# Optimization experiments

Measured on AMD Instinct MI355X. Metric: run time of the kernel, lower is better.

## Reference

```python
import jax, jax.numpy as jnp
import numpy as np

B, N, D, F, L, R = 16, 1024, 256, 128, 2, 2


def setup_inputs() -> dict:
    key = jax.random.key(0)
    ks = jax.random.split(key, 12)
    s = 0.05
    return {
        "node_embed": jax.random.normal(ks[0], (B, N, D), jnp.float32),
        "input_x": jax.random.normal(ks[1], (B, F), jnp.float32),
        "adj": jax.random.randint(ks[2], (R, B, N, N), 0, 2, jnp.int32),
        "WQi_w": jax.random.normal(ks[3], (L, F, F), jnp.float32) * s,
        "WQi_b": jnp.zeros((L, F), jnp.float32),
        "WQ_w": jax.random.normal(ks[4], (L, D + F, D), jnp.float32) * s,
        "WQ_b": jnp.zeros((L, D), jnp.float32),
        "WK_w": jax.random.normal(ks[5], (L, R, D + F, D), jnp.float32) * s,
        "WK_b": jnp.zeros((L, R, D), jnp.float32),
        "WV_w": jax.random.normal(ks[6], (L, R, D + F, D), jnp.float32) * s,
        "WV_b": jnp.zeros((L, R, D), jnp.float32),
        "WF_w": jax.random.normal(ks[7], (L, R * D, D), jnp.float32) * s,
        "WF_b": jnp.zeros((L, D), jnp.float32),
        "ln_g": jnp.ones((L, D), jnp.float32),
        "ln_b": jnp.zeros((L, D), jnp.float32),
    }


def _layer_norm(x, g, b, eps=1e-5):
    mu = jnp.mean(x, axis=-1, keepdims=True)
    var = jnp.var(x, axis=-1, keepdims=True)
    return (x - mu) * jax.lax.rsqrt(var + eps) * g + b


def reference(node_embed, input_x, adj, WQi_w, WQi_b, WQ_w, WQ_b,
              WK_w, WK_b, WV_w, WV_b, WF_w, WF_b, ln_g, ln_b):
    scale = 1.0 / (D ** 0.5)
    h = node_embed
    for l in range(L):
        # input feature projection, broadcast over nodes
        x1 = input_x @ WQi_w[l] + WQi_b[l]              # (B, F)
        x1 = jnp.broadcast_to(x1[:, None, :], (h.shape[0], h.shape[1], F))
        qc = jnp.concatenate([h, x1], axis=-1)          # (B, N, D+F)
        q = qc @ WQ_w[l] + WQ_b[l]                      # (B, N, D)
        outs = []
        for r in range(R):
            k = qc @ WK_w[l, r] + WK_b[l, r]            # (B, N, D)
            v = qc @ WV_w[l, r] + WV_b[l, r]            # (B, N, D)
            scores = jnp.einsum('bnd,bmd->bnm', q, k) * scale
            scores = jnp.where(adj[r] == 0, -1e9, scores)
            alpha = jax.nn.softmax(scores, axis=-1)
            outs.append(jnp.einsum('bnm,bmd->bnd', alpha, v))
        h_concat = jnp.concatenate(outs, axis=-1)       # (B, N, R*D)
        h_fused = jax.nn.relu(h_concat @ WF_w[l] + WF_b[l])
        h = _layer_norm(h + h_fused, ln_g[l], ln_b[l])
    return h
```

## Files before the change

### kernel.cpp

```cpp
#include <hip/hip_runtime.h>
#include <hip/hip_bf16.h>

#define BB 16
#define NN 1024
#define DD 256
#define FF_ 128
#define LL 2
#define RR 2
#define DF 384
#define MM (BB*NN)
#define NPROJ 1280
#define PK 768

typedef __attribute__((ext_vector_type(8))) short s16x8;
typedef __attribute__((ext_vector_type(4))) float f32x4;
typedef __attribute__((ext_vector_type(16))) float f32x16;
typedef __attribute__((ext_vector_type(2))) unsigned int u32x2;
typedef __attribute__((ext_vector_type(4))) unsigned int u32x4;
typedef __attribute__((ext_vector_type(4))) unsigned short us16x4;

__device__ __forceinline__ unsigned short f2bf(float f){
  unsigned u = __builtin_bit_cast(unsigned, f);
  u += 0x7fff + ((u >> 16) & 1);
  return (unsigned short)(u >> 16);
}

__device__ __forceinline__ void gload16(const void* g, void* l){
  __builtin_amdgcn_global_load_lds(
      (const __attribute__((address_space(1))) unsigned int*)g,
      (__attribute__((address_space(3))) unsigned int*)l, 16, 0, 0);
}

#define MFMA16(a,b,c) __builtin_amdgcn_mfma_f32_16x16x32_bf16((a),(b),(c),0,0,0)
#define MFMA32(a,b,c) __builtin_amdgcn_mfma_f32_32x32x16_bf16((a),(b),(c),0,0,0)

__global__ __launch_bounds__(256) void pack_adj(const int* __restrict__ adj,
                                                unsigned long long* __restrict__ bits){
  int w = threadIdx.x >> 6, lane = threadIdx.x & 63;
  size_t row = (size_t)blockIdx.x * 4 + w;
  const int* a = adj + row * NN;
  unsigned long long* brow = bits + row * 16;
  #pragma unroll
  for (int j = 0; j < 16; ++j){
    unsigned long long m = __ballot(a[j*64 + lane] != 0);
    if (lane == 0) brow[j] = m;
  }
}

#define PREP_WT   3840
#define PREP_WTF  1024
#define PREP_BALL 10
#define PREP_X1   16
#define PREP_H    2048
#define PREP_TOT  (PREP_WT+PREP_WTF+PREP_BALL+PREP_X1+PREP_H)

__global__ __launch_bounds__(256) void prep(
    const float* __restrict__ node, const float* __restrict__ inx,
    const float* __restrict__ WQi_w, const float* __restrict__ WQi_b,
    const float* __restrict__ WQ_w, const float* __restrict__ WK_w,
    const float* __restrict__ WV_w, const float* __restrict__ WQ_b,
    const float* __restrict__ WK_b, const float* __restrict__ WV_b,
    const float* __restrict__ WF_w,
    unsigned short* __restrict__ wtall, unsigned short* __restrict__ wtf,
    float* __restrict__ ball, unsigned short* __restrict__ x1bf,
    unsigned short* __restrict__ hbf){
  int bid = blockIdx.x, t = threadIdx.x;
  if (bid < PREP_WT){
    int o = bid*256 + t;
    int l = o / (NPROJ*DF); int oo = o - l*(NPROJ*DF);
    int n = oo / DF, k = oo - n*DF;
    const float* WQ = WQ_w + (size_t)l*DF*256;
    const float* WK = WK_w + (size_t)l*RR*DF*256;
    const float* WV = WV_w + (size_t)l*RR*DF*256;
    float v;
    if (n < 256)      v = WQ[(size_t)k*256 + n];
    else if (n < 768) v = WK[(size_t)((n-256)>>8)*(DF*256) + (size_t)k*256 + ((n-256)&255)];
    else              v = WV[(size_t)((n-768)>>8)*(DF*256) + (size_t)k*256 + ((n-768)&255)];
    wtall[o] = f2bf(v);
  } else if (bid < PREP_WT + PREP_WTF){
    int o = (bid - PREP_WT)*256 + t;
    int l = o >> 17; int oo = o & 131071;
    int n = oo >> 9, k = oo & 511;
    wtf[o] = f2bf(WF_w[(size_t)l*512*256 + (size_t)k*256 + n]);
  } else if (bid < PREP_WT + PREP_WTF + PREP_BALL){
    int o = (bid - PREP_WT - PREP_WTF)*256 + t;
    if (o < 2*NPROJ){
      int l = o / NPROJ, n = o - l*NPROJ;
      float v = (n < 256) ? WQ_b[l*256 + n]
              : (n < 768) ? WK_b[(size_t)l*512 + (n-256)]
                          : WV_b[(size_t)l*512 + (n-768)];
      ball[o] = v;
    }
  } else if (bid < PREP_WT + PREP_WTF + PREP_BALL + PREP_X1){
    int o = (bid - PREP_WT - PREP_WTF - PREP_BALL)*256 + t;
    int l = o >> 11, bj = o & 2047;
    int b = bj >> 7, j = bj & 127;
    const float* w = WQi_w + (size_t)l*FF_*FF_;
    float s = WQi_b[l*FF_ + j];
    for (int i = 0; i < FF_; ++i) s += inx[b*FF_ + i] * w[i*FF_ + j];
    x1bf[o] = f2bf(s);
  } else {
    int o = (bid - (PREP_TOT - PREP_H))*256 + t;
    const float4* src = (const float4*)node + (size_t)o*2;
    float4 a = src[0], c = src[1];
    uint4 pk;
    pk.x = (unsigned)f2bf(a.x) | ((unsigned)f2bf(a.y) << 16);
    pk.y = (unsigned)f2bf(a.z) | ((unsigned)f2bf(a.w) << 16);
    pk.z = (unsigned)f2bf(c.x) | ((unsigned)f2bf(c.y) << 16);
    pk.w = (unsigned)f2bf(c.z) | ((unsigned)f2bf(c.w) << 16);
    *(uint4*)(hbf + (size_t)o*8) = pk;
  }
}

__global__ __launch_bounds__(256) void gemm_big(const unsigned short* __restrict__ hbf,
    const unsigned short* __restrict__ x1l, const unsigned short* __restrict__ Wt,
    const float* __restrict__ bias, unsigned short* __restrict__ POUT,
    unsigned short* __restrict__ vtall){
  __shared__ unsigned short As[2][128*32];
  __shared__ unsigned short Bs[2][128*32];
  int t = threadIdx.x, lane = t & 63, w = t >> 6;
  int wr = w >> 1, wc = w & 1, l15 = lane & 15, lhi = lane >> 4;
  int bm = blockIdx.x, bn = blockIdx.y, bb = bm >> 3;
  f32x4 acc[4][4];
  #pragma unroll
  for (int m = 0; m < 4; ++m)
    #pragma unroll
    for (int n = 0; n < 4; ++n) acc[m][n] = (f32x4){0.f,0.f,0.f,0.f};

  auto STAGE = [&](int bi, int kk){
    #pragma unroll
    for (int i = 0; i < 2; ++i){
      int base = w*2048 + i*1024;
      int off = base + lane*16;
      int row = off >> 6, cb = off & 63;
      const char* asrc = (kk < 8)
        ? (const char*)hbf + ((size_t)(bm*128 + row)*256 + kk*32)*2 + cb
        : (const char*)x1l + ((size_t)bb*128 + (kk-8)*32)*2 + cb;
      gload16(asrc, (char*)As[bi] + base);
      gload16((const char*)Wt + ((size_t)(bn*128 + row)*DF + kk*32)*2 + cb,
              (char*)Bs[bi] + base);
    }
  };

  STAGE(0, 0);
  __syncthreads();
  for (int kk = 0; kk < 12; ++kk){
    int cur = kk & 1;
    if (kk + 1 < 12) STAGE(cur ^ 1, kk + 1);
    s16x8 af[4], bfr[4];
    #pragma unroll
    for (int m = 0; m < 4; ++m) af[m]  = *(const s16x8*)&As[cur][(wr*64 + m*16 + l15)*32 + lhi*8];
    #pragma unroll
    for (int n = 0; n < 4; ++n) bfr[n] = *(const s16x8*)&Bs[cur][(wc*64 + n*16 + l15)*32 + lhi*8];
    __builtin_amdgcn_s_setprio(1);
    #pragma unroll
    for (int m = 0; m < 4; ++m)
      #pragma unroll
      for (int n = 0; n < 4; ++n)
        acc[m][n] = MFMA16(af[m], bfr[n], acc[m][n]);
    __builtin_amdgcn_s_setprio(0);
    __syncthreads();
  }

  if (bn < 6){
    #pragma unroll
    for (int n = 0; n < 4; ++n){
      int gn = bn*128 + wc*64 + n*16 + l15;
      float bv = bias[gn];
      #pragma unroll
      for (int m = 0; m < 4; ++m){
        int gm = bm*128 + wr*64 + m*16 + lhi*4;
        #pragma unroll
        for (int i = 0; i < 4; ++i)
          POUT[(size_t)(gm + i)*PK + gn] = f2bf(acc[m][n][i] + bv);
      }
    }
  } else {
    #pragma unroll
    for (int n = 0; n < 4; ++n){
      int gn = bn*128 + wc*64 + n*16 + l15;
      float bv = bias[gn];
      int rv = gn - 768;
      int r = rv >> 8, d = rv & 255;
      #pragma unroll
      for (int m = 0; m < 4; ++m){
        int mb = (bm & 7)*128 + wr*64 + m*16 + lhi*4;
        us16x4 pk;
        #pragma unroll
        for (int i = 0; i < 4; ++i) pk[i] = f2bf(acc[m][n][i] + bv);
        *(us16x4*)(vtall + ((size_t)((r*16 + bb)*256 + d))*NN + mb) = pk;
      }
    }
  }
}

__global__ __launch_bounds__(256, 1) void attn5(const unsigned short* __restrict__ P,
    const unsigned short* __restrict__ VT, const unsigned long long* __restrict__ bits,
    unsigned short* __restrict__ hc){
  __shared__ char smem[131072];

  int t = threadIdx.x, lane = t & 63, w = t >> 6;
  int h = lane >> 5, l31 = lane & 31;
  int F = blockIdx.x;
  int xcd = F & 7, j = F >> 3;
  int qt = j & 7;
  int gidx = xcd*4 + (j >> 3);
  int b = gidx & 15, r = gidx >> 4;
  const float C = 0.09016844f;

  size_t kcol = 256 + (size_t)r*256;
  const unsigned short* Vb = VT + ((size_t)(r*16 + b))*256*NN;

  int qrow = qt*128 + w*32 + l31;

  s16x8 qf[16];
  {
    const unsigned short* qp = P + ((size_t)(b*NN + qrow))*PK + h*8;
    #pragma unroll
    for (int d_ = 0; d_ < 16; ++d_) qf[d_] = *(const s16x8*)(qp + d_*16);
  }

  f32x16 acc[8];
  #pragma unroll
  for (int dt = 0; dt < 8; ++dt)
    #pragma unroll
    for (int i = 0; i < 16; ++i) acc[dt][i] = 0.f;
  float mrow = -3e38f, lrow = 0.f;
  const unsigned long long* bitp = bits + ((size_t)(r*BB + b)*NN + qrow)*16;

  auto STAGE = [&](int bi, int kt){
    char* Kd = smem + bi*32768;
    char* Vd = smem + 65536 + bi*32768;
    #pragma unroll
    for (int i = 0; i < 8; ++i){
      int base = w*8192 + i*1024;
      int off = base + lane*16;
      int row = off >> 9, cb = off & 511;
      int scb = cb ^ ((row & 7) << 4);
      gload16((const char*)P + ((size_t)(b*NN + kt*64 + row)*PK + kcol)*2 + scb,
              Kd + base);
    }
    #pragma unroll
    for (int i = 0; i < 8; ++i){
      int base = w*8192 + i*1024;
      int off = base + lane*16;
      int row = off >> 7, cb = off & 127;
      int scb = cb ^ ((row & 7) << 4);
      gload16((const char*)Vb + ((size_t)row*NN + kt*64)*2 + scb,
              Vd + base);
    }
  };

  STAGE(0, 0);

  for (int kt = 0; kt < 16; ++kt){
    __builtin_amdgcn_s_barrier();
    unsigned long long mwv = bitp[kt];
    if (kt + 1 < 16){
      STAGE((kt+1)&1, kt+1);
      asm volatile("s_waitcnt vmcnt(16)" ::: "memory");
    } else {
      asm volatile("s_waitcnt vmcnt(0)" ::: "memory");
    }
    __builtin_amdgcn_s_barrier();
    __builtin_amdgcn_sched_barrier(0);

    const char* Kcur = smem + (kt & 1)*32768;
    const char* Vcur = smem + 65536 + (kt & 1)*32768;

    #pragma unroll
    for (int s = 0; s < 2; ++s){
      f32x16 st;
      #pragma unroll
      for (int i = 0; i < 16; ++i) st[i] = 0.f;
      int krow = s*32 + l31;
      int swzk = (krow & 7) << 4;
      const char* kbase = Kcur + krow*512;
      #pragma unroll
      for (int d_ = 0; d_ < 16; ++d_){
        s16x8 kf = *(const s16x8*)(kbase + ((d_*32 + h*16) ^ swzk));
        st = MFMA32(kf, qf[d_], st);
      }

      unsigned mw = (unsigned)(mwv >> (s*32));
      float tm = -3e38f;
      #pragma unroll
      for (int rr = 0; rr < 16; ++rr){
        int kb = (rr & 3) + 8*(rr >> 2) + 4*h;
        float sv = st[rr] * C;
        sv = ((mw >> kb) & 1u) ? sv : -1.443e9f;
        st[rr] = sv;
        tm = fmaxf(tm, sv);
      }
      tm = fmaxf(tm, __shfl_xor(tm, 32));
      if (tm > mrow + 10.f){
        float f = exp2f(mrow - tm);
        mrow = tm;
        lrow *= f;
        #pragma unroll
        for (int dt = 0; dt < 8; ++dt)
          #pragma unroll
          for (int i = 0; i < 16; ++i) acc[dt][i] *= f;
      }
      float rs = 0.f;
      #pragma unroll
      for (int rr = 0; rr < 16; ++rr){
        float e = exp2f(st[rr] - mrow);
        st[rr] = e;
        rs += e;
      }
      rs += __shfl_xor(rs, 32);
      lrow += rs;

      unsigned pk[8];
      #pragma unroll
      for (int p = 0; p < 8; ++p){
        unsigned rpk;
        float lo = st[p*2], hi = st[p*2+1];
        asm("v_cvt_pk_bf16_f32 %0, %1, %2" : "=v"(rpk) : "v"(lo), "v"(hi));
        pk[p] = rpk;
      }
      unsigned sA = h ? pk[0] : pk[2], sB = h ? pk[1] : pk[3];
      unsigned sC = h ? pk[4] : pk[6], sD = h ? pk[5] : pk[7];
      unsigned rxA = (unsigned)__shfl_xor((int)sA, 32);
      unsigned rxB = (unsigned)__shfl_xor((int)sB, 32);
      unsigned rxC = (unsigned)__shfl_xor((int)sC, 32);
      unsigned rxD = (unsigned)__shfl_xor((int)sD, 32);
      u32x4 pv0, pv1;
      pv0[0] = h ? rxA : pk[0]; pv0[1] = h ? rxB : pk[1];
      pv0[2] = h ? pk[2] : rxA; pv0[3] = h ? pk[3] : rxB;
      pv1[0] = h ? rxC : pk[4]; pv1[1] = h ? rxD : pk[5];
      pv1[2] = h ? pk[6] : rxC; pv1[3] = h ? pk[7] : rxD;
      s16x8 pa0 = __builtin_bit_cast(s16x8, pv0);
      s16x8 pa1 = __builtin_bit_cast(s16x8, pv1);

      #pragma unroll
      for (int dt = 0; dt < 8; ++dt){
        int vrow = dt*32 + l31;
        int swzv = (vrow & 7) << 4;
        const char* vbase = Vcur + vrow*128;
        s16x8 vf0 = *(const s16x8*)(vbase + (((2*s)*32 + h*16) ^ swzv));
        acc[dt] = MFMA32(vf0, pa0, acc[dt]);
        s16x8 vf1 = *(const s16x8*)(vbase + (((2*s+1)*32 + h*16) ^ swzv));
        acc[dt] = MFMA32(vf1, pa1, acc[dt]);
      }
    }
  }

  __builtin_amdgcn_s_barrier();
  float inv = 1.f / lrow;
  unsigned short* Ob = (unsigned short*)smem;
  int qloc = w*32 + l31;
  #pragma unroll
  for (int dt = 0; dt < 8; ++dt){
    #pragma unroll
    for (int g = 0; g < 4; ++g){
      float a0 = acc[dt][g*4+0]*inv, a1 = acc[dt][g*4+1]*inv;
      float a2 = acc[dt][g*4+2]*inv, a3 = acc[dt][g*4+3]*inv;
      unsigned r0, r1;
      asm("v_cvt_pk_bf16_f32 %0, %1, %2" : "=v"(r0) : "v"(a0), "v"(a1));
      asm("v_cvt_pk_bf16_f32 %0, %1, %2" : "=v"(r1) : "v"(a2), "v"(a3));
      int d = dt*32 + 8*g + 4*h;
      int byteoff = qloc*512 + ((d*2) ^ ((qloc & 7) << 4));
      u32x2 pv; pv[0] = r0; pv[1] = r1;
      *(u32x2*)((char*)Ob + byteoff) = pv;
    }
  }
  __builtin_amdgcn_s_barrier();
  #pragma unroll
  for (int it = 0; it < 16; ++it){
    int off = (it*256 + t) * 16;
    int row = off >> 9, cb = off & 511;
    int scb = cb ^ ((row & 7) << 4);
    u32x4 v = *(const u32x4*)((char*)Ob + row*512 + scb);
    int q = qt*128 + row;
    *(u32x4*)((char*)hc + (((size_t)(b*NN + q))*512 + r*256 + (cb >> 1))*2) = v;
  }
}

__global__ __launch_bounds__(256) void gemm_ff(const unsigned short* __restrict__ A,
    const unsigned short* __restrict__ Wt, const float* __restrict__ bias,
    float* __restrict__ out){
  __shared__ unsigned short As[2][128*32];
  __shared__ unsigned short Bs[2][128*32];
  int t = threadIdx.x, lane = t & 63, w = t >> 6;
  int wr = w >> 1, wc = w & 1, l15 = lane & 15, lhi = lane >> 4;
  int bm = blockIdx.x, bn = blockIdx.y;
  f32x4 acc[4][4];
  #pragma unroll
  for (int m = 0; m < 4; ++m)
    #pragma unroll
    for (int n = 0; n < 4; ++n) acc[m][n] = (f32x4){0.f,0.f,0.f,0.f};

  auto STAGE = [&](int bi, int kk){
    #pragma unroll
    for (int i = 0; i < 2; ++i){
      int base = w*2048 + i*1024;
      int off = base + lane*16;
      int row = off >> 6, cb = off & 63;
      gload16((const char*)A  + ((size_t)(bm*128 + row)*512 + kk*32)*2 + cb,
              (char*)As[bi] + base);
      gload16((const char*)Wt + ((size_t)(bn*128 + row)*512 + kk*32)*2 + cb,
              (char*)Bs[bi] + base);
    }
  };

  STAGE(0, 0);
  __syncthreads();
  for (int kk = 0; kk < 16; ++kk){
    int cur = kk & 1;
    if (kk + 1 < 16) STAGE(cur ^ 1, kk + 1);
    s16x8 af[4], bfr[4];
    #pragma unroll
    for (int m = 0; m < 4; ++m) af[m]  = *(const s16x8*)&As[cur][(wr*64 + m*16 + l15)*32 + lhi*8];
    #pragma unroll
    for (int n = 0; n < 4; ++n) bfr[n] = *(const s16x8*)&Bs[cur][(wc*64 + n*16 + l15)*32 + lhi*8];
    __builtin_amdgcn_s_setprio(1);
    #pragma unroll
    for (int m = 0; m < 4; ++m)
      #pragma unroll
      for (int n = 0; n < 4; ++n)
        acc[m][n] = MFMA16(af[m], bfr[n], acc[m][n]);
    __builtin_amdgcn_s_setprio(0);
    __syncthreads();
  }

  #pragma unroll
  for (int n = 0; n < 4; ++n){
    int gn = bn*128 + wc*64 + n*16 + l15;
    float bv = bias[gn];
    #pragma unroll
    for (int m = 0; m < 4; ++m){
      int gm = bm*128 + wr*64 + m*16 + lhi*4;
      #pragma unroll
      for (int i = 0; i < 4; ++i)
        out[(size_t)(gm + i)*DD + gn] = acc[m][n][i] + bv;
    }
  }
}

template<int WRITEH>
__global__ __launch_bounds__(256) void ln_res2(const float* __restrict__ ff,
    const float* __restrict__ hin, const float* __restrict__ g,
    const float* __restrict__ bv, float* __restrict__ hout,
    unsigned short* __restrict__ hbf){
  int w = threadIdx.x >> 6, lane = threadIdx.x & 63;
  size_t row = (size_t)blockIdx.x * 4 + w;
  f32x4 fv = *(const f32x4*)(ff  + row*DD + lane*4);
  f32x4 hv = *(const f32x4*)(hin + row*DD + lane*4);
  float x[4], s = 0.f, ss = 0.f;
  #pragma unroll
  for (int j = 0; j < 4; ++j){ x[j] = fmaxf(fv[j], 0.f) + hv[j]; s += x[j]; ss += x[j]*x[j]; }
  #pragma unroll
  for (int xm = 1; xm < 64; xm <<= 1){ s += __shfl_xor(s, xm); ss += __shfl_xor(ss, xm); }
  float mu = s * (1.f/256.f);
  float var = ss * (1.f/256.f) - mu*mu;
  float rstd = rsqrtf(var + 1e-5f);
  f32x4 o;
  #pragma unroll
  for (int j = 0; j < 4; ++j){ int c = lane*4 + j; o[j] = (x[j]-mu)*rstd*g[c] + bv[c]; }
  *(f32x4*)(hout + row*DD + lane*4) = o;
  if (WRITEH){
    uint2 pv;
    pv.x = (unsigned)f2bf(o[0]) | ((unsigned)f2bf(o[1]) << 16);
    pv.y = (unsigned)f2bf(o[2]) | ((unsigned)f2bf(o[3]) << 16);
    *(uint2*)(hbf + row*DD + lane*4) = pv;
  }
}

extern "C" void kernel_launch(void* const* d_in, const int* in_sizes, int n_in,
                              void* d_out, int out_size, void* d_ws, size_t ws_size,
                              hipStream_t stream){
  (void)in_sizes; (void)n_in; (void)out_size; (void)ws_size;
  const float* node  = (const float*)d_in[0];
  const float* inx   = (const float*)d_in[1];
  const int*   adj   = (const int*)d_in[2];
  const float* WQi_w = (const float*)d_in[3];
  const float* WQi_b = (const float*)d_in[4];
  const float* WQ_w  = (const float*)d_in[5];
  const float* WQ_b  = (const float*)d_in[6];
  const float* WK_w  = (const float*)d_in[7];
  const float* WK_b  = (const float*)d_in[8];
  const float* WV_w  = (const float*)d_in[9];
  const float* WV_b  = (const float*)d_in[10];
  const float* WF_w  = (const float*)d_in[11];
  const float* WF_b  = (const float*)d_in[12];
  const float* ln_g  = (const float*)d_in[13];
  const float* ln_b  = (const float*)d_in[14];
  float* hout = (float*)d_out;

  char* wsp = (char*)d_ws;
  auto alloc = [&](size_t n){ char* p = wsp; wsp += (n + 255) & ~(size_t)255; return p; };
  unsigned long long* bits = (unsigned long long*)alloc((size_t)RR*BB*NN*16*8);
  unsigned short* wtall = (unsigned short*)alloc((size_t)2*NPROJ*DF*2);
  unsigned short* wtf   = (unsigned short*)alloc((size_t)2*DD*512*2);
  float*          ball  = (float*)alloc((size_t)2*NPROJ*4);
  unsigned short* x1bf  = (unsigned short*)alloc((size_t)2*BB*FF_*2);
  unsigned short* hbf   = (unsigned short*)alloc((size_t)MM*DD*2);
  unsigned short* POUT  = (unsigned short*)alloc((size_t)MM*PK*2);
  unsigned short* vtall = (unsigned short*)alloc((size_t)RR*BB*DD*NN*2);
  unsigned short* hc    = (unsigned short*)alloc((size_t)MM*512*2);
  float*          ffo   = (float*)alloc((size_t)MM*DD*4);

  pack_adj<<<RR*BB*NN/4, 256, 0, stream>>>(adj, bits);
  prep<<<PREP_TOT, 256, 0, stream>>>(node, inx, WQi_w, WQi_b, WQ_w, WK_w, WV_w,
                                     WQ_b, WK_b, WV_b, WF_w,
                                     wtall, wtf, ball, x1bf, hbf);

  for (int l = 0; l < LL; ++l){
    gemm_big<<<dim3(128,10), 256, 0, stream>>>(hbf, x1bf + (size_t)l*BB*FF_,
        wtall + (size_t)l*NPROJ*DF, ball + (size_t)l*NPROJ, POUT, vtall);

    attn5<<<256, 256, 0, stream>>>(POUT, vtall, bits, hc);

    gemm_ff<<<dim3(128,2), 256, 0, stream>>>(hc, wtf + (size_t)l*DD*512, WF_b + l*DD, ffo);

    if (l == 0) ln_res2<1><<<MM/4, 256, 0, stream>>>(ffo, node, ln_g, ln_b, hout, hbf);
    else        ln_res2<0><<<MM/4, 256, 0, stream>>>(ffo, (const float*)hout,
                                                     ln_g + DD, ln_b + DD, hout, nullptr);
  }
}
```

Baseline: 303.0 us.

## Split key range across two wave groups in attention and merge softmax partials

The attention kernel now runs 512 threads per block. Two groups of four waves each process half of the keys for the same 128 query rows, and their online-softmax partials (accumulators, running max and sum) are merged through shared memory before bf16 output is written directly to global memory. This doubles the waves available to hide latency and halves the sequential key loop. In exchange the double-buffered prefetch is dropped in favour of a load, full wait, then compute pattern each iteration. The launch bounds of (512, 2) may also force register pressure or spilling given the large per-thread accumulator and Q fragment state.

```diff
diff --git a/kernel.cpp b/kernel.cpp
--- a/kernel.cpp
+++ b/kernel.cpp
@@ -194,13 +194,14 @@
   }
 }
 
-__global__ __launch_bounds__(256, 1) void attn5(const unsigned short* __restrict__ P,
+__global__ __launch_bounds__(512, 2) void attn6(const unsigned short* __restrict__ P,
     const unsigned short* __restrict__ VT, const unsigned long long* __restrict__ bits,
     unsigned short* __restrict__ hc){
-  __shared__ char smem[131072];
+  __shared__ char smem[135168];
 
   int t = threadIdx.x, lane = t & 63, w = t >> 6;
   int h = lane >> 5, l31 = lane & 31;
+  int hh = w >> 2, qs = w & 3;
   int F = blockIdx.x;
   int xcd = F & 7, j = F >> 3;
   int qt = j & 7;
@@ -211,7 +212,7 @@
   size_t kcol = 256 + (size_t)r*256;
   const unsigned short* Vb = VT + ((size_t)(r*16 + b))*256*NN;
 
-  int qrow = qt*128 + w*32 + l31;
+  int qrow = qt*128 + qs*32 + l31;
 
   s16x8 qf[16];
   {
@@ -228,45 +229,33 @@
   float mrow = -3e38f, lrow = 0.f;
   const unsigned long long* bitp = bits + ((size_t)(r*BB + b)*NN + qrow)*16;
 
-  auto STAGE = [&](int bi, int kt){
-    char* Kd = smem + bi*32768;
-    char* Vd = smem + 65536 + bi*32768;
+  for (int it = 0; it < 8; ++it){
+    __builtin_amdgcn_s_barrier();
     #pragma unroll
     for (int i = 0; i < 8; ++i){
-      int base = w*8192 + i*1024;
-      int off = base + lane*16;
-      int row = off >> 9, cb = off & 511;
+      int o = i*8192 + w*1024 + lane*16;
+      int hhs = o >> 15, local = o & 32767;
+      int row = local >> 9, cb = local & 511;
       int scb = cb ^ ((row & 7) << 4);
-      gload16((const char*)P + ((size_t)(b*NN + kt*64 + row)*PK + kcol)*2 + scb,
-              Kd + base);
+      gload16((const char*)P + ((size_t)(b*NN + hhs*512 + it*64 + row)*PK + kcol)*2 + scb,
+              smem + o);
     }
     #pragma unroll
     for (int i = 0; i < 8; ++i){
-      int base = w*8192 + i*1024;
-      int off = base + lane*16;
-      int row = off >> 7, cb = off & 127;
-      int scb = cb ^ ((row & 7) << 4);
-      gload16((const char*)Vb + ((size_t)row*NN + kt*64)*2 + scb,
-              Vd + base);
-    }
-  };
-
-  STAGE(0, 0);
-
-  for (int kt = 0; kt < 16; ++kt){
-    __builtin_amdgcn_s_barrier();
-    unsigned long long mwv = bitp[kt];
-    if (kt + 1 < 16){
-      STAGE((kt+1)&1, kt+1);
-      asm volatile("s_waitcnt vmcnt(16)" ::: "memory");
-    } else {
-      asm volatile("s_waitcnt vmcnt(0)" ::: "memory");
-    }
+      int o = i*8192 + w*1024 + lane*16;
+      int hhs = o >> 15, local = o & 32767;
+      int vrow = local >> 7, cb = local & 127;
+      int scb = cb ^ ((vrow & 7) << 4);
+      gload16((const char*)Vb + ((size_t)vrow*NN + hhs*512 + it*64)*2 + scb,
+              smem + 65536 + o);
+    }
+    unsigned long long mwv = bitp[hh*8 + it];
+    asm volatile("s_waitcnt vmcnt(0)" ::: "memory");
     __builtin_amdgcn_s_barrier();
     __builtin_amdgcn_sched_barrier(0);
 
-    const char* Kcur = smem + (kt & 1)*32768;
-    const char* Vcur = smem + 65536 + (kt & 1)*32768;
+    const char* Kcur = smem + hh*32768;
+    const char* Vcur = smem + 65536 + hh*32768;
 
     #pragma unroll
     for (int s = 0; s < 2; ++s){
@@ -348,33 +337,47 @@
   }
 
   __builtin_amdgcn_s_barrier();
-  float inv = 1.f / lrow;
-  unsigned short* Ob = (unsigned short*)smem;
-  int qloc = w*32 + l31;
-  #pragma unroll
-  for (int dt = 0; dt < 8; ++dt){
-    #pragma unroll
-    for (int g = 0; g < 4; ++g){
-      float a0 = acc[dt][g*4+0]*inv, a1 = acc[dt][g*4+1]*inv;
-      float a2 = acc[dt][g*4+2]*inv, a3 = acc[dt][g*4+3]*inv;
-      unsigned r0, r1;
-      asm("v_cvt_pk_bf16_f32 %0, %1, %2" : "=v"(r0) : "v"(a0), "v"(a1));
-      asm("v_cvt_pk_bf16_f32 %0, %1, %2" : "=v"(r1) : "v"(a2), "v"(a3));
-      int d = dt*32 + 8*g + 4*h;
-      int byteoff = qloc*512 + ((d*2) ^ ((qloc & 7) << 4));
-      u32x2 pv; pv[0] = r0; pv[1] = r1;
-      *(u32x2*)((char*)Ob + byteoff) = pv;
-    }
+  if (hh){
+    char* reg = smem + qs*33792 + lane*528;
+    #pragma unroll
+    for (int dt = 0; dt < 8; ++dt)
+      #pragma unroll
+      for (int g = 0; g < 4; ++g){
+        f32x4 v;
+        v[0] = acc[dt][g*4+0]; v[1] = acc[dt][g*4+1];
+        v[2] = acc[dt][g*4+2]; v[3] = acc[dt][g*4+3];
+        *(f32x4*)(reg + (dt*4+g)*16) = v;
+      }
+    *(float*)(reg + 512) = mrow;
+    *(float*)(reg + 516) = lrow;
   }
   __builtin_amdgcn_s_barrier();
-  #pragma unroll
-  for (int it = 0; it < 16; ++it){
-    int off = (it*256 + t) * 16;
-    int row = off >> 9, cb = off & 511;
-    int scb = cb ^ ((row & 7) << 4);
-    u32x4 v = *(const u32x4*)((char*)Ob + row*512 + scb);
-    int q = qt*128 + row;
-    *(u32x4*)((char*)hc + (((size_t)(b*NN + q))*512 + r*256 + (cb >> 1))*2) = v;
+  if (!hh){
+    const char* reg = smem + qs*33792 + lane*528;
+    float m2 = *(const float*)(reg + 512);
+    float l2 = *(const float*)(reg + 516);
+    float m = fmaxf(mrow, m2);
+    float w1 = exp2f(mrow - m), w2 = exp2f(m2 - m);
+    float inv = 1.f / (lrow*w1 + l2*w2);
+    float f1 = w1*inv, f2 = w2*inv;
+    unsigned short* hrow = hc + ((size_t)(b*NN + qrow))*(RR*DD) + r*DD;
+    #pragma unroll
+    for (int dt = 0; dt < 8; ++dt){
+      #pragma unroll
+      for (int g = 0; g < 4; ++g){
+        f32x4 a2 = *(const f32x4*)(reg + (dt*4+g)*16);
+        float a0 = acc[dt][g*4+0]*f1 + a2[0]*f2;
+        float a1 = acc[dt][g*4+1]*f1 + a2[1]*f2;
+        float a2v = acc[dt][g*4+2]*f1 + a2[2]*f2;
+        float a3 = acc[dt][g*4+3]*f1 + a2[3]*f2;
+        unsigned r0, r1;
+        asm("v_cvt_pk_bf16_f32 %0, %1, %2" : "=v"(r0) : "v"(a0), "v"(a1));
+        asm("v_cvt_pk_bf16_f32 %0, %1, %2" : "=v"(r1) : "v"(a2v), "v"(a3));
+        int d = dt*32 + 8*g + 4*h;
+        u32x2 pv; pv[0] = r0; pv[1] = r1;
+        *(u32x2*)(hrow + d) = pv;
+      }
+    }
   }
 }
 
@@ -511,7 +514,7 @@
     gemm_big<<<dim3(128,10), 256, 0, stream>>>(hbf, x1bf + (size_t)l*BB*FF_,
         wtall + (size_t)l*NPROJ*DF, ball + (size_t)l*NPROJ, POUT, vtall);
 
-    attn5<<<256, 256, 0, stream>>>(POUT, vtall, bits, hc);
+    attn6<<<256, 512, 0, stream>>>(POUT, vtall, bits, hc);
 
     gemm_ff<<<dim3(128,2), 256, 0, stream>>>(hc, wtf + (size_t)l*DD*512, WF_b + l*DD, ffo);
 
```

New measurement: 360.3 us. +18.9%, slower.

## Split attention head dim across wave pairs with 512-thread blocks

Applied to the files above, without the earlier changes.

The attention kernel now launches 512 threads per block, with each pair of waves sharing a 32-row query slice and splitting the 256-wide value/output dimension in half. Each wave holds half as many accumulators, and the block has twice as many waves to hide latency. In exchange, QK^T scores and softmax are computed twice, once per wave of a pair. The output is written straight from registers to global memory instead of being staged through shared memory, and the K/V double buffer is now synchronised with a barrier at the end of each iteration.

```diff
diff --git a/kernel.cpp b/kernel.cpp
--- a/kernel.cpp
+++ b/kernel.cpp
@@ -194,13 +194,14 @@
   }
 }
 
-__global__ __launch_bounds__(256, 1) void attn5(const unsigned short* __restrict__ P,
+__global__ __launch_bounds__(512, 1) void attn9(const unsigned short* __restrict__ P,
     const unsigned short* __restrict__ VT, const unsigned long long* __restrict__ bits,
     unsigned short* __restrict__ hc){
   __shared__ char smem[131072];
 
   int t = threadIdx.x, lane = t & 63, w = t >> 6;
   int h = lane >> 5, l31 = lane & 31;
+  int qsub = w >> 1, dh = w & 1;
   int F = blockIdx.x;
   int xcd = F & 7, j = F >> 3;
   int qt = j & 7;
@@ -210,8 +211,7 @@
 
   size_t kcol = 256 + (size_t)r*256;
   const unsigned short* Vb = VT + ((size_t)(r*16 + b))*256*NN;
-
-  int qrow = qt*128 + w*32 + l31;
+  int qrow = qt*128 + qsub*32 + l31;
 
   s16x8 qf[16];
   {
@@ -219,54 +219,52 @@
     #pragma unroll
     for (int d_ = 0; d_ < 16; ++d_) qf[d_] = *(const s16x8*)(qp + d_*16);
   }
-
-  f32x16 acc[8];
-  #pragma unroll
-  for (int dt = 0; dt < 8; ++dt)
+  asm volatile("s_waitcnt vmcnt(0)" ::: "memory");
+
+  f32x16 acc[4];
+  #pragma unroll
+  for (int dt = 0; dt < 4; ++dt)
     #pragma unroll
     for (int i = 0; i < 16; ++i) acc[dt][i] = 0.f;
   float mrow = -3e38f, lrow = 0.f;
   const unsigned long long* bitp = bits + ((size_t)(r*BB + b)*NN + qrow)*16;
 
-  auto STAGE = [&](int bi, int kt){
-    char* Kd = smem + bi*32768;
-    char* Vd = smem + 65536 + bi*32768;
-    #pragma unroll
-    for (int i = 0; i < 8; ++i){
-      int base = w*8192 + i*1024;
-      int off = base + lane*16;
-      int row = off >> 9, cb = off & 511;
-      int scb = cb ^ ((row & 7) << 4);
-      gload16((const char*)P + ((size_t)(b*NN + kt*64 + row)*PK + kcol)*2 + scb,
-              Kd + base);
-    }
-    #pragma unroll
-    for (int i = 0; i < 8; ++i){
-      int base = w*8192 + i*1024;
-      int off = base + lane*16;
-      int row = off >> 7, cb = off & 127;
-      int scb = cb ^ ((row & 7) << 4);
-      gload16((const char*)Vb + ((size_t)row*NN + kt*64)*2 + scb,
-              Vd + base);
+  auto STAGE = [&](int buf, int kt){
+    char* base = smem + buf*65536;
+    #pragma unroll
+    for (int i = 0; i < 4; ++i){
+      int o = i*8192 + t*16;
+      int kr = o >> 9, cb = o & 511;
+      int lcb = cb ^ ((kr & 7) << 4);
+      gload16((const char*)P + ((size_t)(b*NN + kt*64 + kr)*PK + kcol)*2 + lcb,
+              base + o);
+    }
+    #pragma unroll
+    for (int i = 0; i < 4; ++i){
+      int o = i*8192 + t*16;
+      int vr = o >> 7, cb = o & 127;
+      int lcb = cb ^ ((vr & 7) << 4);
+      gload16((const char*)Vb + ((size_t)vr*NN + kt*64)*2 + lcb,
+              base + 32768 + o);
     }
   };
 
   STAGE(0, 0);
 
   for (int kt = 0; kt < 16; ++kt){
-    __builtin_amdgcn_s_barrier();
-    unsigned long long mwv = bitp[kt];
+    int cur = kt & 1;
+    unsigned long long mwv64 = bitp[kt];
     if (kt + 1 < 16){
-      STAGE((kt+1)&1, kt+1);
-      asm volatile("s_waitcnt vmcnt(16)" ::: "memory");
+      STAGE(cur ^ 1, kt + 1);
+      asm volatile("s_waitcnt vmcnt(8)" ::: "memory");
     } else {
       asm volatile("s_waitcnt vmcnt(0)" ::: "memory");
     }
     __builtin_amdgcn_s_barrier();
     __builtin_amdgcn_sched_barrier(0);
 
-    const char* Kcur = smem + (kt & 1)*32768;
-    const char* Vcur = smem + 65536 + (kt & 1)*32768;
+    const char* Kc = smem + cur*65536;
+    const char* Vc = smem + cur*65536 + 32768;
 
     #pragma unroll
     for (int s = 0; s < 2; ++s){
@@ -275,14 +273,14 @@
       for (int i = 0; i < 16; ++i) st[i] = 0.f;
       int krow = s*32 + l31;
       int swzk = (krow & 7) << 4;
-      const char* kbase = Kcur + krow*512;
+      const char* kbase = Kc + krow*512;
       #pragma unroll
       for (int d_ = 0; d_ < 16; ++d_){
         s16x8 kf = *(const s16x8*)(kbase + ((d_*32 + h*16) ^ swzk));
         st = MFMA32(kf, qf[d_], st);
       }
 
-      unsigned mw = (unsigned)(mwv >> (s*32));
+      unsigned mw = (unsigned)(mwv64 >> (s*32));
       float tm = -3e38f;
       #pragma unroll
       for (int rr = 0; rr < 16; ++rr){
@@ -298,7 +296,7 @@
         mrow = tm;
         lrow *= f;
         #pragma unroll
-        for (int dt = 0; dt < 8; ++dt)
+        for (int dt = 0; dt < 4; ++dt)
           #pragma unroll
           for (int i = 0; i < 16; ++i) acc[dt][i] *= f;
       }
@@ -335,24 +333,24 @@
       s16x8 pa1 = __builtin_bit_cast(s16x8, pv1);
 
       #pragma unroll
-      for (int dt = 0; dt < 8; ++dt){
-        int vrow = dt*32 + l31;
-        int swzv = (vrow & 7) << 4;
-        const char* vbase = Vcur + vrow*128;
+      for (int dt = 0; dt < 4; ++dt){
+        int vr = dh*128 + dt*32 + l31;
+        int swzv = (vr & 7) << 4;
+        const char* vbase = Vc + vr*128;
         s16x8 vf0 = *(const s16x8*)(vbase + (((2*s)*32 + h*16) ^ swzv));
         acc[dt] = MFMA32(vf0, pa0, acc[dt]);
         s16x8 vf1 = *(const s16x8*)(vbase + (((2*s+1)*32 + h*16) ^ swzv));
         acc[dt] = MFMA32(vf1, pa1, acc[dt]);
       }
     }
-  }
-
-  __builtin_amdgcn_s_barrier();
+
+    __builtin_amdgcn_s_barrier();
+  }
+
   float inv = 1.f / lrow;
-  unsigned short* Ob = (unsigned short*)smem;
-  int qloc = w*32 + l31;
-  #pragma unroll
-  for (int dt = 0; dt < 8; ++dt){
+  unsigned short* hrow = hc + ((size_t)(b*NN + qrow))*(RR*DD) + r*DD;
+  #pragma unroll
+  for (int dt = 0; dt < 4; ++dt){
     #pragma unroll
     for (int g = 0; g < 4; ++g){
       float a0 = acc[dt][g*4+0]*inv, a1 = acc[dt][g*4+1]*inv;
@@ -360,21 +358,10 @@
       unsigned r0, r1;
       asm("v_cvt_pk_bf16_f32 %0, %1, %2" : "=v"(r0) : "v"(a0), "v"(a1));
       asm("v_cvt_pk_bf16_f32 %0, %1, %2" : "=v"(r1) : "v"(a2), "v"(a3));
-      int d = dt*32 + 8*g + 4*h;
-      int byteoff = qloc*512 + ((d*2) ^ ((qloc & 7) << 4));
+      int d = dh*128 + dt*32 + 8*g + 4*h;
       u32x2 pv; pv[0] = r0; pv[1] = r1;
-      *(u32x2*)((char*)Ob + byteoff) = pv;
-    }
-  }
-  __builtin_amdgcn_s_barrier();
-  #pragma unroll
-  for (int it = 0; it < 16; ++it){
-    int off = (it*256 + t) * 16;
-    int row = off >> 9, cb = off & 511;
-    int scb = cb ^ ((row & 7) << 4);
-    u32x4 v = *(const u32x4*)((char*)Ob + row*512 + scb);
-    int q = qt*128 + row;
-    *(u32x4*)((char*)hc + (((size_t)(b*NN + q))*512 + r*256 + (cb >> 1))*2) = v;
+      *(u32x2*)(hrow + d) = pv;
+    }
   }
 }
 
@@ -511,7 +498,7 @@
     gemm_big<<<dim3(128,10), 256, 0, stream>>>(hbf, x1bf + (size_t)l*BB*FF_,
         wtall + (size_t)l*NPROJ*DF, ball + (size_t)l*NPROJ, POUT, vtall);
 
-    attn5<<<256, 256, 0, stream>>>(POUT, vtall, bits, hc);
+    attn9<<<256, 512, 0, stream>>>(POUT, vtall, bits, hc);
 
     gemm_ff<<<dim3(128,2), 256, 0, stream>>>(hc, wtf + (size_t)l*DD*512, WF_b + l*DD, ffo);
 
```

New measurement: 302.3 us. About the same (-0.2%).
